# Optimization experiments

Hardware: AMD Instinct MI355X
Metric: run time of the kernel (lower is better)

Reference implementation:

```python
import jax, jax.numpy as jnp
import numpy as np

B, S, D, H = 2, 2048, 1024, 16
HD = D // H


def setup_inputs() -> dict:
    key = jax.random.key(0)
    ks = jax.random.split(key, 16)
    sc = 0.02
    return {
        "hidden_states": jax.random.normal(ks[0], (B, S, D), jnp.float32),
        "Wq": jax.random.normal(ks[1], (D, D), jnp.float32) * sc,
        "bq": jnp.zeros((D,), jnp.float32),
        "Wk": jax.random.normal(ks[2], (D, D), jnp.float32) * sc,
        "bk": jnp.zeros((D,), jnp.float32),
        "Wv": jax.random.normal(ks[3], (D, D), jnp.float32) * sc,
        "bv": jnp.zeros((D,), jnp.float32),
        "Wo": jax.random.normal(ks[4], (D, D), jnp.float32) * sc,
        "bo": jnp.zeros((D,), jnp.float32),
        "rel_W": jax.random.normal(ks[5], (3, 2 * D), jnp.float32) * sc,
        "rel_b": jnp.zeros((3,), jnp.float32),
        "logical_bias": jax.random.normal(ks[6], (H, 3), jnp.float32) * sc,
        "gate_W": jax.random.normal(ks[7], (H, D), jnp.float32) * sc,
        "gate_b": jnp.zeros((H,), jnp.float32),
    }


def reference(hidden_states, Wq, bq, Wk, bk, Wv, bv, Wo, bo,
              rel_W, rel_b, logical_bias, gate_W, gate_b):
    x = hidden_states
    b, s, d = x.shape
    h = gate_W.shape[0]
    hd = d // h
    scale = hd ** 0.5

    q = (x @ Wq.T + bq).reshape(b, s, h, hd)
    k = (x @ Wk.T + bk).reshape(b, s, h, hd)
    v = (x @ Wv.T + bv).reshape(b, s, h, hd)

    # [b, h, i, j] raw attention scores
    attn_scores = jnp.einsum('bihd,bjhd->bhij', q, k) / scale

    # Pairwise relation logits WITHOUT materializing the [b,s,s,2d] concat:
    # cat([h_i, h_j]) @ W.T == h_i @ W[:, :d].T + h_j @ W[:, d:].T
    li = x @ rel_W[:, :d].T   # (b, s, 3) contribution from position i
    lj = x @ rel_W[:, d:].T   # (b, s, 3) contribution from position j
    logits = li[:, :, None, :] + lj[:, None, :, :] + rel_b  # (b, s, s, 3)
    relation_probs = jax.nn.softmax(logits, axis=-1)

    bias = jnp.einsum('bijk,hk->bhij', relation_probs, logical_bias)

    gate = jax.nn.sigmoid(x @ gate_W.T + gate_b)        # (b, s, h)
    gate = jnp.transpose(gate, (0, 2, 1))[..., None]    # (b, h, s, 1)

    attn_scores = attn_scores + gate * bias
    attn_weights = jax.nn.softmax(attn_scores, axis=-1)

    out = jnp.einsum('bhij,bjhd->bihd', attn_weights, v).reshape(b, s, d)
    return out @ Wo.T + bo
```

## Files before the change

### kernel.cpp

```cpp
#include <hip/hip_runtime.h>
#include <math.h>

#define B_   2
#define S_   2048
#define D_   1024
#define H_   16
#define NROW (B_ * S_)
#define L2E_ 1.4426950408889634f

typedef __bf16 bf16_t;
typedef __bf16 bf16x8 __attribute__((ext_vector_type(8)));
typedef __bf16 bf16x4v __attribute__((ext_vector_type(4)));
typedef float  f32x4  __attribute__((ext_vector_type(4)));

#define MFMA16(a, b, c) __builtin_amdgcn_mfma_f32_16x16x32_bf16((a), (b), (c), 0, 0, 0)

#if __has_builtin(__builtin_amdgcn_exp2f)
#define EXP2F(x) __builtin_amdgcn_exp2f(x)
#else
#define EXP2F(x) exp2f(x)
#endif

__device__ __forceinline__ void glds16(const void* src, void* lds) {
    __builtin_amdgcn_global_load_lds(
        (const __attribute__((address_space(1))) void*)src,
        (__attribute__((address_space(3))) void*)lds, 16, 0, 0);
}

__global__ __launch_bounds__(256)
void cvt_all(const float* __restrict__ x, const float* __restrict__ wq,
             const float* __restrict__ wk, const float* __restrict__ wv,
             const float* __restrict__ wo, bf16_t* __restrict__ xb,
             bf16_t* __restrict__ wqb, bf16_t* __restrict__ wkb,
             bf16_t* __restrict__ wvb, bf16_t* __restrict__ wob) {
    int bid = blockIdx.x;
    const float* src;
    bf16_t* dst;
    int base;
    if (bid < 4096) { src = x; dst = xb; base = bid; }
    else {
        int k = (bid - 4096) >> 10;
        base = (bid - 4096) & 1023;
        src = (k == 0) ? wq : (k == 1) ? wk : (k == 2) ? wv : wo;
        dst = (k == 0) ? wqb : (k == 1) ? wkb : (k == 2) ? wvb : wob;
    }
    int idx = base * 1024 + threadIdx.x * 4;
    float4 v = *(const float4*)&src[idx];
    bf16x4v o;
    o[0] = (bf16_t)v.x; o[1] = (bf16_t)v.y; o[2] = (bf16_t)v.z; o[3] = (bf16_t)v.w;
    *(bf16x4v*)&dst[idx] = o;
}

__global__ __launch_bounds__(256)
void proj_small(const float* __restrict__ x, const float* __restrict__ relW,
                const float* __restrict__ relB, const float* __restrict__ gateW,
                const float* __restrict__ gateB,
                float* __restrict__ EA4, float* __restrict__ EB4,
                float* __restrict__ GA) {
    const int wave = threadIdx.x >> 6;
    const int lane = threadIdx.x & 63;
    const int row  = blockIdx.x * 4 + wave;

    const float* xr = x + (size_t)row * D_;
    float xv[16];
    #pragma unroll
    for (int t = 0; t < 16; ++t) xv[t] = xr[lane + 64 * t];

    for (int c = 0; c < 22; ++c) {
        const float* w;
        if (c < 3)       w = relW + c * (2 * D_);
        else if (c < 6)  w = relW + (c - 3) * (2 * D_) + D_;
        else             w = gateW + (size_t)(c - 6) * D_;
        float s = 0.f;
        #pragma unroll
        for (int t = 0; t < 16; ++t) s += xv[t] * w[lane + 64 * t];
        #pragma unroll
        for (int off = 32; off; off >>= 1) s += __shfl_xor(s, off);
        if (lane == 0) {
            if (c < 3)      EA4[row * 4 + c] = expf(s + relB[c]);
            else if (c < 6) EB4[row * 4 + (c - 3)] = expf(s);
            else            GA[row * H_ + (c - 6)] =
                                1.f / (1.f + expf(-(s + gateB[c - 6])));
        }
    }
}

__device__ __forceinline__ void gemm_body128(
    const bf16_t* __restrict__ A, const bf16_t* __restrict__ W,
    const float* __restrict__ bias, float scale, int row0, int col0,
    bf16_t* As, bf16_t* Bs, int outbf16, void* Cout, int N, int K)
{
    const int tid = threadIdx.x, w = tid >> 6, l = tid & 63;
    const int wr = w >> 1, wc = w & 1, p16 = l & 15, g4 = l >> 4;

    f32x4 acc[4][4];
    #pragma unroll
    for (int i = 0; i < 4; ++i)
        #pragma unroll
        for (int j = 0; j < 4; ++j) acc[i][j] = (f32x4){0.f, 0.f, 0.f, 0.f};

    const int sr = l >> 3, sc = l & 7;
    const bf16_t* aS = A + (size_t)(row0 + w * 32) * K;
    const bf16_t* bS = W + (size_t)(col0 + w * 32) * K;

    for (int k0 = 0; k0 < K; k0 += 64) {
        #pragma unroll
        for (int i = 0; i < 4; ++i) {
            int r = i * 8 + sr;
            int co = k0 + ((sc ^ sr) << 3);
            glds16(aS + (size_t)r * K + co, As + (w * 32 + i * 8) * 64);
            glds16(bS + (size_t)r * K + co, Bs + (w * 32 + i * 8) * 64);
        }
        __syncthreads();
        #pragma unroll
        for (int c = 0; c < 2; ++c) {
            bf16x8 af[4], bfr[4];
            #pragma unroll
            for (int mi = 0; mi < 4; ++mi) {
                int row = wr * 64 + mi * 16 + p16;
                af[mi] = *(const bf16x8*)&As[row * 64 + (((c * 4 + g4) ^ (row & 7)) << 3)];
            }
            #pragma unroll
            for (int nj = 0; nj < 4; ++nj) {
                int row = wc * 64 + nj * 16 + p16;
                bfr[nj] = *(const bf16x8*)&Bs[row * 64 + (((c * 4 + g4) ^ (row & 7)) << 3)];
            }
            #pragma unroll
            for (int mi = 0; mi < 4; ++mi)
                #pragma unroll
                for (int nj = 0; nj < 4; ++nj)
                    acc[mi][nj] = MFMA16(af[mi], bfr[nj], acc[mi][nj]);
        }
        __syncthreads();
    }

    const int cj = col0 + wc * 64 + p16;
    #pragma unroll
    for (int nj = 0; nj < 4; ++nj) {
        int j = cj + nj * 16;
        float bj = bias[j];
        #pragma unroll
        for (int mi = 0; mi < 4; ++mi) {
            int ib = row0 + wr * 64 + mi * 16 + g4 * 4;
            #pragma unroll
            for (int r = 0; r < 4; ++r) {
                float v = (acc[mi][nj][r] + bj) * scale;
                if (outbf16)
                    ((bf16_t*)Cout)[(size_t)(ib + r) * N + j] = (bf16_t)v;
                else
                    ((float*)Cout)[(size_t)(ib + r) * N + j] = v;
            }
        }
    }
}

__global__ __launch_bounds__(256)
void gemm_qkv(const bf16_t* __restrict__ xb,
              const bf16_t* __restrict__ wq, const bf16_t* __restrict__ wk,
              const bf16_t* __restrict__ wv,
              const float* __restrict__ bq, const float* __restrict__ bk,
              const float* __restrict__ bv,
              bf16_t* __restrict__ Qb, bf16_t* __restrict__ Kb,
              bf16_t* __restrict__ Vb) {
    __shared__ __align__(16) bf16_t As[128 * 64];
    __shared__ __align__(16) bf16_t Bs[128 * 64];
    const int seg = blockIdx.x >> 3;
    const int col0 = (blockIdx.x & 7) * 128;
    const int row0 = blockIdx.y * 128;
    const bf16_t* W = (seg == 0) ? wq : (seg == 1) ? wk : wv;
    const float* bias = (seg == 0) ? bq : (seg == 1) ? bk : bv;
    bf16_t* C = (seg == 0) ? Qb : (seg == 1) ? Kb : Vb;
    const float scale = (seg == 0) ? 0.125f * L2E_ : 1.0f;
    gemm_body128(xb, W, bias, scale, row0, col0, As, Bs, 1, C, D_, D_);
}

__global__ __launch_bounds__(256)
void gemm_out(const bf16_t* __restrict__ A, const bf16_t* __restrict__ wo,
              const float* __restrict__ bo, float* __restrict__ out) {
    __shared__ __align__(16) bf16_t As[128 * 64];
    __shared__ __align__(16) bf16_t Bs[128 * 64];
    gemm_body128(A, wo, bo, 1.0f, blockIdx.y * 128, blockIdx.x * 128,
                 As, Bs, 0, out, D_, D_);
}

__global__ __launch_bounds__(256)
void flash_mfma(const bf16_t* __restrict__ Q, const bf16_t* __restrict__ Kg,
                const bf16_t* __restrict__ Vg, const float4* __restrict__ EA4,
                const float4* __restrict__ EB4, const float* __restrict__ GA,
                const float* __restrict__ LB, bf16_t* __restrict__ AO) {
    __shared__ __align__(16) bf16_t Ks[64 * 64];
    __shared__ __align__(16) bf16_t Vt[64 * 64];
    __shared__ __align__(16) bf16_t Ps[4][16 * 64];
    __shared__ __align__(16) float  ebs[64 * 4];

    const int tid = threadIdx.x, w = tid >> 6, l = tid & 63;
    const int b = blockIdx.y >> 4, h = blockIdx.y & 15;
    const int i0 = blockIdx.x * 64;
    const size_t rowb = (size_t)b * S_ + i0;
    const int p16 = l & 15, g4 = l >> 4;

    const float lb0 = LB[h * 3 + 0], lb1 = LB[h * 3 + 1], lb2 = LB[h * 3 + 2];

    bf16x8 qf[2];
    {
        const bf16_t* qp = Q + (rowb + w * 16 + p16) * D_ + h * 64 + g4 * 8;
        qf[0] = *(const bf16x8*)qp;
        qf[1] = *(const bf16x8*)(qp + 32);
    }

    bf16x8 zer;
    #pragma unroll
    for (int u = 0; u < 8; ++u) zer[u] = (bf16_t)0.f;
    bf16x8 cnf = zer, eaf = zer;
    {
        size_t gi = rowb + w * 16 + p16;
        float4 e = EA4[gi];
        float g = GA[gi * H_ + h] * L2E_;
        if (g4 == 0) {
            cnf[0] = (bf16_t)(g * e.x * lb0);
            cnf[1] = (bf16_t)(g * e.y * lb1);
            cnf[2] = (bf16_t)(g * e.z * lb2);
            eaf[0] = (bf16_t)e.x;
            eaf[1] = (bf16_t)e.y;
            eaf[2] = (bf16_t)e.z;
        }
    }

    float lsum[4] = {0.f, 0.f, 0.f, 0.f};
    f32x4 o[4];
    #pragma unroll
    for (int nb = 0; nb < 4; ++nb) o[nb] = (f32x4){0.f, 0.f, 0.f, 0.f};

    const int vj = tid >> 2, vc = (tid & 3) * 16;
    const int kr0 = l >> 3, kc0 = l & 7;

    for (int j0 = 0; j0 < S_; j0 += 64) {
        const size_t jb = (size_t)b * S_ + j0;
        {
            int rowA = w * 16 + kr0;
            int rowB = rowA + 8;
            glds16(Kg + (jb + rowA) * D_ + h * 64 + ((kc0 ^ (rowA & 7)) << 3),
                   Ks + w * 1024);
            glds16(Kg + (jb + rowB) * D_ + h * 64 + ((kc0 ^ (rowB & 7)) << 3),
                   Ks + w * 1024 + 512);
        }
        bf16x8 v0, v1;
        {
            const bf16_t* vp = Vg + (jb + vj) * D_ + h * 64 + vc;
            v0 = *(const bf16x8*)vp;
            v1 = *(const bf16x8*)(vp + 8);
        }
        if (tid < 64) *(float4*)&ebs[tid * 4] = EB4[jb + tid];
        #pragma unroll
        for (int u = 0; u < 8; ++u) {
            int hd = vc + u;
            int sw = ((hd & 7) ^ ((hd >> 3) & 7)) << 3;
            Vt[hd * 64 + (vj ^ sw)] = v0[u];
        }
        #pragma unroll
        for (int u = 0; u < 8; ++u) {
            int hd = vc + 8 + u;
            int sw = ((hd & 7) ^ ((hd >> 3) & 7)) << 3;
            Vt[hd * 64 + (vj ^ sw)] = v1[u];
        }
        __syncthreads();

        f32x4 nacc[4], dacc[4];
        #pragma unroll
        for (int nb = 0; nb < 4; ++nb) {
            float4 e = *(const float4*)&ebs[(nb * 16 + p16) * 4];
            bf16x8 ebf = zer;
            if (g4 == 0) {
                ebf[0] = (bf16_t)e.x; ebf[1] = (bf16_t)e.y; ebf[2] = (bf16_t)e.z;
            }
            f32x4 z4 = (f32x4){0.f, 0.f, 0.f, 0.f};
            nacc[nb] = MFMA16(cnf, ebf, z4);
            dacc[nb] = MFMA16(eaf, ebf, z4);
        }

        f32x4 s[4];
        #pragma unroll
        for (int nb = 0; nb < 4; ++nb) {
            s[nb] = (f32x4){0.f, 0.f, 0.f, 0.f};
            int row = nb * 16 + p16;
            int sw = row & 7;
            bf16x8 k0v = *(const bf16x8*)&Ks[row * 64 + ((g4    ) ^ sw) * 8];
            bf16x8 k1v = *(const bf16x8*)&Ks[row * 64 + ((g4 + 4) ^ sw) * 8];
            s[nb] = MFMA16(qf[0], k0v, s[nb]);
            s[nb] = MFMA16(qf[1], k1v, s[nb]);
        }

        #pragma unroll
        for (int nb = 0; nb < 4; ++nb) {
            #pragma unroll
            for (int r = 0; r < 4; ++r) {
                float sv = s[nb][r] + nacc[nb][r] * __builtin_amdgcn_rcpf(dacc[nb][r]);
                float p = EXP2F(sv);
                bf16_t pb = (bf16_t)p;
                lsum[r] += (float)pb;
                int irow = g4 * 4 + r;
                int jcol = nb * 16 + p16;
                Ps[w][irow * 64 + (jcol ^ ((irow & 7) << 3))] = pb;
            }
        }

        bf16x8 pf0, pf1;
        {
            int sw = p16 & 7;
            pf0 = *(const bf16x8*)&Ps[w][p16 * 64 + ((g4    ) ^ sw) * 8];
            pf1 = *(const bf16x8*)&Ps[w][p16 * 64 + ((g4 + 4) ^ sw) * 8];
        }
        #pragma unroll
        for (int nb = 0; nb < 4; ++nb) {
            int vrow = nb * 16 + p16;
            int sw = (vrow & 7) ^ ((vrow >> 3) & 7);
            bf16x8 vf0 = *(const bf16x8*)&Vt[vrow * 64 + ((g4    ) ^ sw) * 8];
            bf16x8 vf1 = *(const bf16x8*)&Vt[vrow * 64 + ((g4 + 4) ^ sw) * 8];
            o[nb] = MFMA16(pf0, vf0, o[nb]);
            o[nb] = MFMA16(pf1, vf1, o[nb]);
        }
        __syncthreads();
    }

    #pragma unroll
    for (int r = 0; r < 4; ++r) {
        float t = lsum[r];
        t += __shfl_xor(t, 1); t += __shfl_xor(t, 2);
        t += __shfl_xor(t, 4); t += __shfl_xor(t, 8);
        lsum[r] = 1.f / t;
    }
    #pragma unroll
    for (int nb = 0; nb < 4; ++nb)
        #pragma unroll
        for (int r = 0; r < 4; ++r) {
            size_t gi = rowb + w * 16 + g4 * 4 + r;
            AO[gi * D_ + h * 64 + nb * 16 + p16] = (bf16_t)(o[nb][r] * lsum[r]);
        }
}

extern "C" void kernel_launch(void* const* d_in, const int* in_sizes, int n_in,
                              void* d_out, int out_size, void* d_ws, size_t ws_size,
                              hipStream_t stream) {
    const float* x    = (const float*)d_in[0];
    const float* Wq   = (const float*)d_in[1];
    const float* bq   = (const float*)d_in[2];
    const float* Wk   = (const float*)d_in[3];
    const float* bk   = (const float*)d_in[4];
    const float* Wv   = (const float*)d_in[5];
    const float* bv   = (const float*)d_in[6];
    const float* Wo   = (const float*)d_in[7];
    const float* bo   = (const float*)d_in[8];
    const float* relW = (const float*)d_in[9];
    const float* relB = (const float*)d_in[10];
    const float* lb   = (const float*)d_in[11];
    const float* gW   = (const float*)d_in[12];
    const float* gb   = (const float*)d_in[13];

    uint8_t* W8 = (uint8_t*)d_ws;
    bf16_t* xb  = (bf16_t*)(W8);
    bf16_t* wqb = (bf16_t*)(W8 + (8u  << 20));
    bf16_t* wkb = (bf16_t*)(W8 + (10u << 20));
    bf16_t* wvb = (bf16_t*)(W8 + (12u << 20));
    bf16_t* wob = (bf16_t*)(W8 + (14u << 20));
    bf16_t* Qb  = (bf16_t*)(W8 + (16u << 20));
    bf16_t* Kb  = (bf16_t*)(W8 + (24u << 20));
    bf16_t* Vb  = (bf16_t*)(W8 + (32u << 20));
    bf16_t* AOb = (bf16_t*)(W8 + (40u << 20));
    float*  EA  = (float*)(W8 + (48u << 20));
    float*  EB  = (float*)(W8 + (48u << 20) + NROW * 16);
    float*  GAp = (float*)(W8 + (48u << 20) + NROW * 32);

    cvt_all<<<8192, 256, 0, stream>>>(x, Wq, Wk, Wv, Wo, xb, wqb, wkb, wvb, wob);
    proj_small<<<NROW / 4, 256, 0, stream>>>(x, relW, relB, gW, gb, EA, EB, GAp);

    gemm_qkv<<<dim3(24, 32), 256, 0, stream>>>(xb, wqb, wkb, wvb, bq, bk, bv,
                                               Qb, Kb, Vb);

    flash_mfma<<<dim3(S_ / 64, B_ * H_), 256, 0, stream>>>(
        Qb, Kb, Vb, (const float4*)EA, (const float4*)EB, GAp, lb, AOb);

    gemm_out<<<dim3(8, 32), 256, 0, stream>>>(AOb, wob, bo, (float*)d_out);
}
```

Baseline: 298.2 us.

## Double-buffer K/V tiles in flash attention and vectorize small projections

The flash attention loop now double-buffers the K, V-transpose and EB tiles in LDS. The next K tile is staged asynchronously and the V tile after it is prefetched into registers two iterations ahead, so global load latency overlaps with the MFMA work of the current tile. Launch bounds are raised to request 3 blocks per CU, and proj_small now uses float4 loads for x and the weights. The cost is twice the LDS for K and V, higher register pressure from the prefetched V values, and possible spills under the occupancy hint.

```diff
diff --git a/kernel.cpp b/kernel.cpp
--- a/kernel.cpp
+++ b/kernel.cpp
@@ -61,19 +61,23 @@
     const int lane = threadIdx.x & 63;
     const int row  = blockIdx.x * 4 + wave;
 
-    const float* xr = x + (size_t)row * D_;
-    float xv[16];
-    #pragma unroll
-    for (int t = 0; t < 16; ++t) xv[t] = xr[lane + 64 * t];
+    const float4* xr = (const float4*)(x + (size_t)row * D_);
+    float4 xv[4];
+    #pragma unroll
+    for (int t = 0; t < 4; ++t) xv[t] = xr[lane + 64 * t];
 
     for (int c = 0; c < 22; ++c) {
         const float* w;
         if (c < 3)       w = relW + c * (2 * D_);
         else if (c < 6)  w = relW + (c - 3) * (2 * D_) + D_;
         else             w = gateW + (size_t)(c - 6) * D_;
+        const float4* w4 = (const float4*)w;
         float s = 0.f;
         #pragma unroll
-        for (int t = 0; t < 16; ++t) s += xv[t] * w[lane + 64 * t];
+        for (int t = 0; t < 4; ++t) {
+            float4 wv = w4[lane + 64 * t];
+            s += xv[t].x * wv.x + xv[t].y * wv.y + xv[t].z * wv.z + xv[t].w * wv.w;
+        }
         #pragma unroll
         for (int off = 32; off; off >>= 1) s += __shfl_xor(s, off);
         if (lane == 0) {
@@ -183,15 +187,15 @@
                  As, Bs, 0, out, D_, D_);
 }
 
-__global__ __launch_bounds__(256)
+__global__ __launch_bounds__(256, 3)
 void flash_mfma(const bf16_t* __restrict__ Q, const bf16_t* __restrict__ Kg,
                 const bf16_t* __restrict__ Vg, const float4* __restrict__ EA4,
                 const float4* __restrict__ EB4, const float* __restrict__ GA,
                 const float* __restrict__ LB, bf16_t* __restrict__ AO) {
-    __shared__ __align__(16) bf16_t Ks[64 * 64];
-    __shared__ __align__(16) bf16_t Vt[64 * 64];
-    __shared__ __align__(16) bf16_t Ps[4][16 * 64];
-    __shared__ __align__(16) float  ebs[64 * 4];
+    __shared__ __align__(16) bf16_t Ks[2][4096];
+    __shared__ __align__(16) bf16_t Vt[2][4096];
+    __shared__ __align__(16) bf16_t Ps[4][1024];
+    __shared__ __align__(16) float  ebs[2][256];
 
     const int tid = threadIdx.x, w = tid >> 6, l = tid & 63;
     const int b = blockIdx.y >> 4, h = blockIdx.y & 15;
@@ -226,49 +230,64 @@
         }
     }
 
+    const int vj = tid >> 2, vc = (tid & 3) * 16;
+    const int kr0 = l >> 3, kc0 = l & 7;
+    const size_t koff1 = (size_t)(w * 16 + kr0) * D_ + ((kc0 ^ kr0) << 3);
+    const size_t koff2 = koff1 + 8 * D_;
+
+    bf16x8 v0, v1;
+    float4 ebr;
+
+#define LOADV(jt) do {                                                         \
+        const size_t jb0 = (size_t)b * S_ + (jt);                              \
+        const bf16_t* vp = Vg + (jb0 + vj) * D_ + h * 64 + vc;                 \
+        v0 = *(const bf16x8*)vp;                                               \
+        v1 = *(const bf16x8*)(vp + 8);                                         \
+        if (tid < 64) ebr = EB4[jb0 + tid];                                    \
+    } while (0)
+
+#define WRITEV(buf) do {                                                       \
+        _Pragma("unroll")                                                      \
+        for (int u = 0; u < 8; ++u) {                                          \
+            int hd = vc + u;                                                   \
+            int sw = ((hd & 7) ^ ((hd >> 3) & 7)) << 3;                        \
+            Vt[buf][hd * 64 + (vj ^ sw)] = v0[u];                              \
+        }                                                                      \
+        _Pragma("unroll")                                                      \
+        for (int u = 0; u < 8; ++u) {                                          \
+            int hd = vc + 8 + u;                                               \
+            int sw = ((hd & 7) ^ ((hd >> 3) & 7)) << 3;                        \
+            Vt[buf][hd * 64 + (vj ^ sw)] = v1[u];                              \
+        }                                                                      \
+        if (tid < 64) *(float4*)&ebs[buf][tid * 4] = ebr;                      \
+    } while (0)
+
+#define STAGEK(buf, jt) do {                                                   \
+        const size_t jbase = (size_t)(b * S_ + (jt)) * D_ + h * 64;            \
+        glds16(Kg + jbase + koff1, &Ks[buf][w * 1024]);                        \
+        glds16(Kg + jbase + koff2, &Ks[buf][w * 1024 + 512]);                  \
+    } while (0)
+
     float lsum[4] = {0.f, 0.f, 0.f, 0.f};
     f32x4 o[4];
     #pragma unroll
     for (int nb = 0; nb < 4; ++nb) o[nb] = (f32x4){0.f, 0.f, 0.f, 0.f};
 
-    const int vj = tid >> 2, vc = (tid & 3) * 16;
-    const int kr0 = l >> 3, kc0 = l & 7;
-
-    for (int j0 = 0; j0 < S_; j0 += 64) {
-        const size_t jb = (size_t)b * S_ + j0;
-        {
-            int rowA = w * 16 + kr0;
-            int rowB = rowA + 8;
-            glds16(Kg + (jb + rowA) * D_ + h * 64 + ((kc0 ^ (rowA & 7)) << 3),
-                   Ks + w * 1024);
-            glds16(Kg + (jb + rowB) * D_ + h * 64 + ((kc0 ^ (rowB & 7)) << 3),
-                   Ks + w * 1024 + 512);
-        }
-        bf16x8 v0, v1;
-        {
-            const bf16_t* vp = Vg + (jb + vj) * D_ + h * 64 + vc;
-            v0 = *(const bf16x8*)vp;
-            v1 = *(const bf16x8*)(vp + 8);
-        }
-        if (tid < 64) *(float4*)&ebs[tid * 4] = EB4[jb + tid];
-        #pragma unroll
-        for (int u = 0; u < 8; ++u) {
-            int hd = vc + u;
-            int sw = ((hd & 7) ^ ((hd >> 3) & 7)) << 3;
-            Vt[hd * 64 + (vj ^ sw)] = v0[u];
-        }
-        #pragma unroll
-        for (int u = 0; u < 8; ++u) {
-            int hd = vc + 8 + u;
-            int sw = ((hd & 7) ^ ((hd >> 3) & 7)) << 3;
-            Vt[hd * 64 + (vj ^ sw)] = v1[u];
-        }
-        __syncthreads();
+    LOADV(0);
+    STAGEK(0, 0);
+    WRITEV(0);
+    LOADV(64);
+    __syncthreads();
+
+    for (int t = 0; t < 32; ++t) {
+        const int cur = t & 1;
+        if (t < 31) { WRITEV(cur ^ 1); STAGEK(cur ^ 1, (t + 1) * 64); }
+        if (t < 30) LOADV((t + 2) * 64);
 
         f32x4 nacc[4], dacc[4];
         #pragma unroll
         for (int nb = 0; nb < 4; ++nb) {
-            float4 e = *(const float4*)&ebs[(nb * 16 + p16) * 4];
+            float4 e = *(const float4*)&ebs[cur][(nb * 16 + p16) * 4];
             bf16x8 ebf = zer;
             if (g4 == 0) {
                 ebf[0] = (bf16_t)e.x; ebf[1] = (bf16_t)e.y; ebf[2] = (bf16_t)e.z;
@@ -284,8 +303,8 @@
             s[nb] = (f32x4){0.f, 0.f, 0.f, 0.f};
             int row = nb * 16 + p16;
             int sw = row & 7;
-            bf16x8 k0v = *(const bf16x8*)&Ks[row * 64 + ((g4    ) ^ sw) * 8];
-            bf16x8 k1v = *(const bf16x8*)&Ks[row * 64 + ((g4 + 4) ^ sw) * 8];
+            bf16x8 k0v = *(const bf16x8*)&Ks[cur][row * 64 + ((g4    ) ^ sw) * 8];
+            bf16x8 k1v = *(const bf16x8*)&Ks[cur][row * 64 + ((g4 + 4) ^ sw) * 8];
             s[nb] = MFMA16(qf[0], k0v, s[nb]);
             s[nb] = MFMA16(qf[1], k1v, s[nb]);
         }
@@ -314,13 +333,16 @@
         for (int nb = 0; nb < 4; ++nb) {
             int vrow = nb * 16 + p16;
             int sw = (vrow & 7) ^ ((vrow >> 3) & 7);
-            bf16x8 vf0 = *(const bf16x8*)&Vt[vrow * 64 + ((g4    ) ^ sw) * 8];
-            bf16x8 vf1 = *(const bf16x8*)&Vt[vrow * 64 + ((g4 + 4) ^ sw) * 8];
+            bf16x8 vf0 = *(const bf16x8*)&Vt[cur][vrow * 64 + ((g4    ) ^ sw) * 8];
+            bf16x8 vf1 = *(const bf16x8*)&Vt[cur][vrow * 64 + ((g4 + 4) ^ sw) * 8];
             o[nb] = MFMA16(pf0, vf0, o[nb]);
             o[nb] = MFMA16(pf1, vf1, o[nb]);
         }
         __syncthreads();
     }
+#undef LOADV
+#undef WRITEV
+#undef STAGEK
 
     #pragma unroll
     for (int r = 0; r < 4; ++r) {
@@ -367,8 +389,8 @@
     bf16_t* Vb  = (bf16_t*)(W8 + (32u << 20));
     bf16_t* AOb = (bf16_t*)(W8 + (40u << 20));
     float*  EA  = (float*)(W8 + (48u << 20));
-    float*  EB  = (float*)(W8 + (48u << 20) + NROW * 16);
-    float*  GAp = (float*)(W8 + (48u << 20) + NROW * 32);
+    float*  EB  = (float*)(W8 + (48u << 20) + 65536);
+    float*  GAp = (float*)(W8 + (48u << 20) + 131072);
 
     cvt_all<<<8192, 256, 0, stream>>>(x, Wq, Wk, Wv, Wo, xb, wqb, wkb, wvb, wob);
     proj_small<<<NROW / 4, 256, 0, stream>>>(x, relW, relB, gW, gb, EA, EB, GAp);
```

New measurement: 281.6 us. 5.6% less time.
